# Optimization experiments

Measured on AMD Instinct MI355X. Metric: run time of the kernel, lower is better.

The kernel has to match this reference:

```python
import jax, jax.numpy as jnp
import numpy as np

N = 9
DIM = 2 ** N  # 512
RANGES = [1, 2, 3]  # PennyLane StronglyEntanglingLayers default: (l % (N-1)) + 1


def _cnot_mat(c, t):
    # CNOT on (control c, target t); wire 0 = most significant bit (default.qubit)
    idx = np.arange(DIM)
    bit = (idx >> (N - 1 - c)) & 1
    new = idx ^ (bit << (N - 1 - t))
    m = np.zeros((DIM, DIM), np.complex64)
    m[new, idx] = 1.0
    return m


def _layer_cnot_ring(r):
    # product of CNOT(i, (i+r) % N) applied for i = 0..N-1 (in circuit order)
    m = np.eye(DIM, dtype=np.complex64)
    for i in range(N):
        m = _cnot_mat(i, (i + r) % N) @ m
    return jnp.asarray(m)


_CNOT_LAYERS = [_layer_cnot_ring(r) for r in RANGES]

# PauliZ diagonal per wire: zd[w, k] = +1/-1 depending on bit w of basis index k
_ZDIAG = jnp.asarray(
    1.0 - 2.0 * (((np.arange(DIM)[None, :] >> (N - 1 - np.arange(N)[:, None])) & 1)),
    dtype=jnp.float32,
)


def _rot2x2(phi, theta, omega):
    # PennyLane Rot = RZ(omega) RY(theta) RZ(phi)
    phi = phi.astype(jnp.complex64)
    theta = theta.astype(jnp.complex64)
    omega = omega.astype(jnp.complex64)
    c = jnp.cos(theta / 2)
    s = jnp.sin(theta / 2)
    m00 = jnp.exp(-0.5j * (phi + omega)) * c
    m01 = -jnp.exp(0.5j * (phi - omega)) * s
    m10 = jnp.exp(-0.5j * (phi - omega)) * s
    m11 = jnp.exp(0.5j * (phi + omega)) * c
    return jnp.stack([jnp.stack([m00, m01]), jnp.stack([m10, m11])])


def _circuit_unitary(weights):
    # Full 512x512 unitary for the 3 StronglyEntanglingLayers (weight-dependent part)
    u = jnp.eye(DIM, dtype=jnp.complex64)
    for l in range(weights.shape[0]):
        rot = _rot2x2(weights[l, 0, 0], weights[l, 0, 1], weights[l, 0, 2])
        for w in range(1, N):
            rot = jnp.kron(rot, _rot2x2(weights[l, w, 0], weights[l, w, 1], weights[l, w, 2]))
        u = _CNOT_LAYERS[l] @ (rot @ u)
    return u


def _forward(x, weights):
    b = x.shape[0]
    # AngleEmbedding (RX) on |0>: per-qubit state [cos(t/2), -i sin(t/2)]
    half = x.astype(jnp.float32) / 2
    q = jnp.stack(
        [jnp.cos(half).astype(jnp.complex64), (-1j) * jnp.sin(half).astype(jnp.complex64)],
        axis=-1,
    )  # [B, 9, 2]
    s = q[:, 0, :]
    for w in range(1, N):  # batched kron across qubits -> [B, 512]
        s = (s[:, :, None] * q[:, w, None, :]).reshape(b, -1)
    u = _circuit_unitary(weights)
    psi = s @ u.T  # [B, 512]
    probs = psi.real ** 2 + psi.imag ** 2  # [B, 512] float32
    return probs @ _ZDIAG.T  # [B, 9] <Z_w> expectations


def setup_inputs() -> dict:
    key = jax.random.key(0)
    k1, k2 = jax.random.split(key)
    return {
        "x": jax.random.normal(k1, (32768, 9), dtype=jnp.float32),
        "weights": jax.random.normal(k2, (3, 9, 3), dtype=jnp.float32),
    }


def reference(x, weights):
    return _forward(x, weights).astype(jnp.float32)
```

## Files before the change

### kernel.cpp

```cpp
#include <hip/hip_runtime.h>
#include <hip/hip_fp16.h>


typedef float v2f __attribute__((ext_vector_type(2)));
typedef _Float16 v2h __attribute__((ext_vector_type(2)));

constexpr int pf(int l, int i) {
    const int r = l + 1; int j = i;
    for (int c = 0; c < 9; ++c) {
        const int bit = (j >> (8 - c)) & 1;
        const int t = (c + r) % 9;
        j ^= bit << (8 - t);
    }
    return j;
}

struct PMask { int m[2][9]; };
constexpr PMask make_pmask() {
    PMask pm{};
    for (int bd = 0; bd < 2; ++bd)
        for (int q = 0; q < 9; ++q) {
            const int img = pf(bd, 1 << q);
            for (int p = 0; p < 9; ++p)
                if ((img >> p) & 1) pm.m[bd][p] |= 1 << q;
        }
    return pm;
}
constexpr PMask PM = make_pmask();

struct Sig3 {
    int wbasis[6];
    int koff[8];
    int rimg[6];
};
constexpr Sig3 make_sig3(int l) {
    Sig3 out{};
    for (int limit = 2; limit <= 64; limit *= 2) {
        for (int idx = 0; idx < 720; ++idx) {
            int pool[6] = {3, 4, 5, 6, 7, 8};
            int perm[6] = {};
            int f = idx;
            const int fact[6] = {120, 24, 6, 2, 1, 1};
            int n = 6;
            for (int pos = 0; pos < 6; ++pos) {
                const int sel = f / fact[pos]; f %= fact[pos];
                perm[pos] = pool[sel];
                for (int m2 = sel; m2 + 1 < n; ++m2) pool[m2] = pool[m2 + 1];
                --n;
            }
            int img[9] = {0, 1, 2, perm[0], perm[1], perm[2],
                          perm[3], perm[4], perm[5]};
            int cnt[32] = {};
            bool ok = true;
            for (int L = 0; L < 64 && ok; ++L) {
                const int j = pf(l, L);
                int addr = 0;
                for (int bb = 0; bb < 9; ++bb)
                    if ((j >> bb) & 1) addr ^= 1 << img[bb];
                if (++cnt[addr & 31] > limit) ok = false;
            }
            if (ok) {
                for (int b2 = 0; b2 < 6; ++b2) {
                    const int j = pf(l, 1 << b2); int v = 0;
                    for (int bb = 0; bb < 9; ++bb)
                        if ((j >> bb) & 1) v ^= 1 << img[bb];
                    out.wbasis[b2] = v;
                }
                for (int k = 0; k < 8; ++k) {
                    const int j = pf(l, k << 6); int v = 0;
                    for (int bb = 0; bb < 9; ++bb)
                        if ((j >> bb) & 1) v ^= 1 << img[bb];
                    out.koff[k] = v;
                }
                for (int b2 = 0; b2 < 6; ++b2) out.rimg[b2] = img[3 + b2];
                return out;
            }
        }
    }
    return out;
}
constexpr Sig3 S3_0 = make_sig3(0);
constexpr Sig3 S3_1 = make_sig3(1);

#define PI_F    3.14159265358979323846f
#define INV2PI  0.15915494309189535f

static __device__ inline unsigned pack_rn(float x, float y) {
    const __half2 h = __floats2half2_rn(x, y);
    return *(const unsigned*)&h;
}

__global__ __launch_bounds__(512) void qtab_kernel(
        const float* __restrict__ wt, float* __restrict__ ws) {
    const int j = threadIdx.x;
    unsigned* wu = (unsigned*)ws;
    if (j < 27) {
        float s, c; __sincosf(0.5f * wt[j * 3 + 1], &s, &c);
        wu[j] = pack_rn(c, s);
    }
    #pragma unroll
    for (int bd = 0; bd < 2; ++bd) {
        float alpha = 0.0f;
        #pragma unroll
        for (int p = 0; p < 9; ++p) {
            const int w = 8 - p;
            const float om = wt[(bd * 9 + w) * 3 + 2];
            const float ph = wt[((bd + 1) * 9 + w) * 3 + 0];
            alpha += ((j >> p) & 1) ? 0.5f * om : -0.5f * om;
            alpha += (__popc(j & PM.m[bd][p]) & 1) ? 0.5f * ph : -0.5f * ph;
        }
        float sn, cs; __sincosf(alpha, &sn, &cs);
        wu[64 + bd * 512 + j] = pack_rn(cs, sn);
    }
    {
        float a = 0.0f;
        #pragma unroll
        for (int p = 0; p < 9; ++p) {
            const int w = 8 - p;
            const float phi = wt[w * 3 + 0];
            a += ((j >> p) & 1) ? (0.5f * phi - 0.5f * PI_F) : (-0.5f * phi);
        }
        float sn, cs; __sincosf(a, &sn, &cs);
        ((v2f*)(ws + 1088))[j] = (v2f){cs, sn};
    }
}

#define APPLY_GATE(G, KB)                                                     \
    {                                                                         \
        _Pragma("unroll")                                                     \
        for (int k0 = 0; k0 < 8; ++k0) if (!(k0 & (KB))) {                    \
            const int k1 = k0 | (KB);                                         \
            unsigned t;                                                       \
            asm("v_pk_mul_f16 %0, %1, %2 op_sel:[0,1] op_sel_hi:[1,1] "       \
                "neg_lo:[0,1] neg_hi:[0,1]"                                   \
                : "=v"(t) : "v"(a[k1]), "s"(G));               \
            asm("v_pk_mul_f16 %0, %0, %1 op_sel:[0,0] op_sel_hi:[1,0]"        \
                : "+v"(a[k1]) : "s"(G));                       \
            asm("v_pk_fma_f16 %0, %1, %2, %0 op_sel:[0,1,0] op_sel_hi:[1,1,1]"\
                : "+v"(a[k1]) : "v"(a[k0]), "s"(G));          \
            asm("v_pk_fma_f16 %0, %0, %1, %2 op_sel:[0,0,0] op_sel_hi:[1,0,1]"\
                : "+v"(a[k0]) : "s"(G), "v"(t));             \
        }                                                                     \
    }

__global__ __launch_bounds__(256) void qsim_kernel(
        const float* __restrict__ x,
        const float* __restrict__ tab,
        float* __restrict__ out,
        int batch) {
    __shared__ uint4 st4[4][128];

    const int tid  = threadIdx.x;
    const int wv   = tid >> 6;
    const int lane = tid & 63;
    const int b    = blockIdx.x * 4 + wv;
    if (b >= batch) return;
    const int bu   = __builtin_amdgcn_readfirstlane(b);

    unsigned* __restrict__ S  = (unsigned*)st4[wv];
    const uint4* __restrict__ S4 = st4[wv];
    const unsigned* __restrict__ tu = (const unsigned*)tab;
    const unsigned* __restrict__ D0 = tu + 64;
    const unsigned* __restrict__ D1 = tu + 576;
    const float4*  __restrict__ PH4 = (const float4*)(tab + 1088);

    float cx[9], sx[9];
    #pragma unroll
    for (int w = 0; w < 9; ++w) {
        const float rev = x[bu * 9 + w] * (0.5f * INV2PI);
        sx[w] = __builtin_amdgcn_sinf(rev);
        cx[w] = __builtin_amdgcn_cosf(rev);
    }
    float P = 1.0f;
    #pragma unroll
    for (int w = 0; w < 6; ++w)
        P *= ((lane >> (5 - w)) & 1) ? sx[w] : cx[w];

    float mk[8];
    {
        const float m0 = P * cx[6],  m1 = P * sx[6];
        const float m00 = m0 * cx[7], m01 = m0 * sx[7];
        const float m10 = m1 * cx[7], m11 = m1 * sx[7];
        mk[0] = m00 * cx[8]; mk[1] = m00 * sx[8];
        mk[2] = m01 * cx[8]; mk[3] = m01 * sx[8];
        mk[4] = m10 * cx[8]; mk[5] = m10 * sx[8];
        mk[6] = m11 * cx[8]; mk[7] = m11 * sx[8];
    }
    unsigned a[8];
    #pragma unroll
    for (int j2 = 0; j2 < 4; ++j2) {
        const float4 ph = PH4[(lane << 2) + j2];
        a[2 * j2]     = pack_rn(ph.x * mk[2 * j2],     ph.y * mk[2 * j2]);
        a[2 * j2 + 1] = pack_rn(ph.z * mk[2 * j2 + 1], ph.w * mk[2 * j2 + 1]);
    }

    const int wb1 = (lane & 31) | ((lane & 32) << 3);
    const int rb1 = ((lane & 7) << 5) | (lane & 0x18) | ((lane & 32) << 3);
    const int wb2 = ((lane >> 3) & 7) | ((lane & 3) << 3) | ((lane & 4) << 6);
    const int rb2 = ((lane & 3) << 3) | ((lane & 4) << 6) | ((lane & 0x38) << 2);
    int t3b[2], rb3[2];
    #pragma unroll
    for (int l = 0; l < 2; ++l) {
        int tb = 0, rb = 0;
        #pragma unroll
        for (int bb = 0; bb < 6; ++bb) {
            const int on = (lane >> bb) & 1;
            tb ^= on ? (l ? S3_1.wbasis[bb] : S3_0.wbasis[bb]) : 0;
            rb ^= on ? (1 << (l ? S3_1.rimg[bb] : S3_0.rimg[bb])) : 0;
        }
        t3b[l] = tb; rb3[l] = rb;
    }

    #pragma unroll
    for (int l = 0; l < 3; ++l) {
        unsigned g[9];
        #pragma unroll
        for (int q = 0; q < 9; ++q) g[q] = tu[l * 9 + q];

        APPLY_GATE(g[6], 4);
        APPLY_GATE(g[7], 2);
        APPLY_GATE(g[8], 1);

        #pragma unroll
        for (int k = 0; k < 8; ++k) S[wb1 + (k << 5)] = a[k];
        {
            const uint4 r0 = S4[(rb1 >> 2)];
            const uint4 r1 = S4[(rb1 >> 2) + 1];
            a[0] = r0.x; a[1] = r0.y; a[2] = r0.z; a[3] = r0.w;
            a[4] = r1.x; a[5] = r1.y; a[6] = r1.z; a[7] = r1.w;
        }

        APPLY_GATE(g[3], 4);
        APPLY_GATE(g[4], 2);
        APPLY_GATE(g[5], 1);

        #pragma unroll
        for (int k = 0; k < 8; ++k) S[wb2 + (k << 5)] = a[k];
        {
            const uint4 r0 = S4[(rb2 >> 2)];
            const uint4 r1 = S4[(rb2 >> 2) + 1];
            a[0] = r0.x; a[1] = r0.y; a[2] = r0.z; a[3] = r0.w;
            a[4] = r1.x; a[5] = r1.y; a[6] = r1.z; a[7] = r1.w;
        }

        APPLY_GATE(g[0], 4);
        APPLY_GATE(g[1], 2);
        APPLY_GATE(g[2], 1);

        if (l < 2) {
            const unsigned* __restrict__ D = (l == 0) ? D0 : D1;
            #pragma unroll
            for (int k = 0; k < 8; ++k) {
                const unsigned d = D[(k << 6) | lane];
                unsigned t;
                asm("v_pk_mul_f16 %0, %1, %2 op_sel:[1,1] op_sel_hi:[0,1] "
                    "neg_lo:[0,1]"
                    : "=v"(t) : "v"(a[k]), "v"(d));
                asm("v_pk_fma_f16 %0, %1, %2, %3 op_sel:[0,0,0] op_sel_hi:[1,0,1]"
                    : "=v"(a[k]) : "v"(a[k]), "v"(d), "v"(t));
            }
            #pragma unroll
            for (int k = 0; k < 8; ++k)
                S[t3b[l] ^ (l ? S3_1.koff[k] : S3_0.koff[k])] = a[k];
            {
                const uint4 r0 = S4[(rb3[l] >> 2)];
                const uint4 r1 = S4[(rb3[l] >> 2) + 1];
                a[0] = r0.x; a[1] = r0.y; a[2] = r0.z; a[3] = r0.w;
                a[4] = r1.x; a[5] = r1.y; a[6] = r1.z; a[7] = r1.w;
            }
        }
    }

    float A0 = 0.f, A1 = 0.f, A2 = 0.f, A3 = 0.f;
    #pragma unroll
    for (int k = 0; k < 8; ++k) {
#if __has_builtin(__builtin_amdgcn_fdot2)
        v2h h, hn;
        { unsigned u = a[k];               h = *(const v2h*)&u; }
        { unsigned un = a[k] ^ 0x80008000u; hn = *(const v2h*)&un; }
        A0 = __builtin_amdgcn_fdot2(h, h, A0, false);
        A1 = __builtin_amdgcn_fdot2(h, (k & 4) ? hn : h, A1, false);
        A2 = __builtin_amdgcn_fdot2(h, (k & 2) ? hn : h, A2, false);
        A3 = __builtin_amdgcn_fdot2(h, (k & 1) ? hn : h, A3, false);
#else
        const __half2 h = *(const __half2*)&a[k];
        const float2 f = __half22float2(h);
        const float p = f.x * f.x + f.y * f.y;
        A0 += p;
        A1 += (k & 4) ? -p : p;
        A2 += (k & 2) ? -p : p;
        A3 += (k & 1) ? -p : p;
#endif
    }
    v2f F01 = (v2f){A0, A1};
    v2f F23 = (v2f){A2, A3};

    #pragma unroll
    for (int d = 1; d < 64; d <<= 1) {
        const float sg1 = (lane & d) ? -1.0f : 1.0f;
        const v2f sgn = (v2f){sg1, sg1};
        v2f p01, p23;
        p01.x = __shfl_xor(F01.x, d, 64);  p01.y = __shfl_xor(F01.y, d, 64);
        p23.x = __shfl_xor(F23.x, d, 64);  p23.y = __shfl_xor(F23.y, d, 64);
        F01 = F01 * sgn + p01;
        F23 = F23 * sgn + p23;
    }
    float* Sf = (float*)S;
    Sf[2 * lane]           = F01.x;
    Sf[2 * lane + 1]       = F01.y;
    Sf[128 + 2 * lane]     = F23.x;
    Sf[128 + 2 * lane + 1] = F23.y;
    if (lane < 9) {
        const int idx = (lane == 0) ? 72  : (lane == 1) ? 36  : (lane == 2) ? 18
                      : (lane == 3) ? 65  : (lane == 4) ? 160 : (lane == 5) ? 145
                      : (lane == 6) ? 73  : (lane == 7) ? 164 : 147;
        out[bu * 9 + lane] = Sf[idx];
    }
}

extern "C" void kernel_launch(void* const* d_in, const int* in_sizes, int n_in,
                              void* d_out, int out_size, void* d_ws, size_t ws_size,
                              hipStream_t stream) {
    const float* x  = (const float*)d_in[0];
    const float* wt = (const float*)d_in[1];
    float* out = (float*)d_out;
    const int batch = in_sizes[0] / 9;
    float* ws = (float*)d_ws;

    hipLaunchKernelGGL(qtab_kernel, dim3(1), dim3(512), 0, stream, wt, ws);
    hipLaunchKernelGGL(qsim_kernel, dim3((batch + 3) / 4), dim3(256), 0, stream,
                       x, ws, out, batch);
}
```

Measured before the change: 99.58 us.

## Process two batch rows per wavefront with interleaved gate and transpose phases

Each wavefront now simulates two batch samples, interleaving gate application of one state with the LDS transpose of the other to expose instruction-level parallelism. The diagonal phase tables are loaded into registers once per wave and reused for both samples, and the grid is halved. This raises register pressure and halves the number of waves, which may reduce occupancy or latency hiding.

```diff
diff --git a/kernel.cpp b/kernel.cpp
--- a/kernel.cpp
+++ b/kernel.cpp
@@ -125,7 +125,7 @@
     }
 }
 
-#define APPLY_GATE(G, KB)                                                     \
+#define APPLY_GATE(ar, G, KB)                                                 \
     {                                                                         \
         _Pragma("unroll")                                                     \
         for (int k0 = 0; k0 < 8; ++k0) if (!(k0 & (KB))) {                    \
@@ -133,13 +133,79 @@
             unsigned t;                                                       \
             asm("v_pk_mul_f16 %0, %1, %2 op_sel:[0,1] op_sel_hi:[1,1] "       \
                 "neg_lo:[0,1] neg_hi:[0,1]"                                   \
-                : "=v"(t) : "v"(a[k1]), "s"(G));               \
+                : "=v"(t) : "v"(ar[k1]), "s"(G));              \
             asm("v_pk_mul_f16 %0, %0, %1 op_sel:[0,0] op_sel_hi:[1,0]"        \
-                : "+v"(a[k1]) : "s"(G));                       \
+                : "+v"(ar[k1]) : "s"(G));                      \
             asm("v_pk_fma_f16 %0, %1, %2, %0 op_sel:[0,1,0] op_sel_hi:[1,1,1]"\
-                : "+v"(a[k1]) : "v"(a[k0]), "s"(G));          \
+                : "+v"(ar[k1]) : "v"(ar[k0]), "s"(G));        \
             asm("v_pk_fma_f16 %0, %0, %1, %2 op_sel:[0,0,0] op_sel_hi:[1,0,1]"\
-                : "+v"(a[k0]) : "s"(G), "v"(t));             \
+                : "+v"(ar[k0]) : "s"(G), "v"(t));            \
+        }                                                                     \
+    }
+
+#define XPOSE(ar, wb, rb)                                                     \
+    {                                                                         \
+        _Pragma("unroll")                                                     \
+        for (int k = 0; k < 8; ++k) S[(wb) + (k << 5)] = ar[k];               \
+        const uint4 r0 = S4[((rb) >> 2)];                                     \
+        const uint4 r1 = S4[((rb) >> 2) + 1];                                 \
+        ar[0] = r0.x; ar[1] = r0.y; ar[2] = r0.z; ar[3] = r0.w;               \
+        ar[4] = r1.x; ar[5] = r1.y; ar[6] = r1.z; ar[7] = r1.w;               \
+    }
+
+#define XPOSE3(ar, ll)                                                        \
+    {                                                                         \
+        _Pragma("unroll")                                                     \
+        for (int k = 0; k < 8; ++k)                                           \
+            S[t3b[ll] ^ ((ll) ? S3_1.koff[k] : S3_0.koff[k])] = ar[k];        \
+        const uint4 r0 = S4[(rb3[ll] >> 2)];                                  \
+        const uint4 r1 = S4[(rb3[ll] >> 2) + 1];                              \
+        ar[0] = r0.x; ar[1] = r0.y; ar[2] = r0.z; ar[3] = r0.w;               \
+        ar[4] = r1.x; ar[5] = r1.y; ar[6] = r1.z; ar[7] = r1.w;               \
+    }
+
+#define CMUL_D(ar, dv)                                                        \
+    {                                                                         \
+        _Pragma("unroll")                                                     \
+        for (int k = 0; k < 8; ++k) {                                         \
+            const unsigned d = dv[k];                                         \
+            unsigned t;                                                       \
+            asm("v_pk_mul_f16 %0, %1, %2 op_sel:[1,1] op_sel_hi:[0,1] "       \
+                "neg_lo:[0,1]"                                                \
+                : "=v"(t) : "v"(ar[k]), "v"(d));                              \
+            asm("v_pk_fma_f16 %0, %1, %2, %3 op_sel:[0,0,0] op_sel_hi:[1,0,1]"\
+                : "=v"(ar[k]) : "v"(ar[k]), "v"(d), "v"(t));                  \
+        }                                                                     \
+    }
+
+#define INIT_STATE(ar, row)                                                   \
+    {                                                                         \
+        float cx[9], sx[9];                                                   \
+        _Pragma("unroll")                                                     \
+        for (int w = 0; w < 9; ++w) {                                         \
+            const float rev = x[(row) * 9 + w] * (0.5f * INV2PI);             \
+            sx[w] = __builtin_amdgcn_sinf(rev);                               \
+            cx[w] = __builtin_amdgcn_cosf(rev);                               \
+        }                                                                     \
+        float P = 1.0f;                                                       \
+        _Pragma("unroll")                                                     \
+        for (int w = 0; w < 6; ++w)                                           \
+            P *= ((lane >> (5 - w)) & 1) ? sx[w] : cx[w];                     \
+        float mk[8];                                                          \
+        {                                                                     \
+            const float m0 = P * cx[6],  m1 = P * sx[6];                      \
+            const float m00 = m0 * cx[7], m01 = m0 * sx[7];                   \
+            const float m10 = m1 * cx[7], m11 = m1 * sx[7];                   \
+            mk[0] = m00 * cx[8]; mk[1] = m00 * sx[8];                         \
+            mk[2] = m01 * cx[8]; mk[3] = m01 * sx[8];                         \
+            mk[4] = m10 * cx[8]; mk[5] = m10 * sx[8];                         \
+            mk[6] = m11 * cx[8]; mk[7] = m11 * sx[8];                         \
+        }                                                                     \
+        _Pragma("unroll")                                                     \
+        for (int j2 = 0; j2 < 4; ++j2) {                                      \
+            const float4 ph = PH4[(lane << 2) + j2];                          \
+            ar[2 * j2]     = pack_rn(ph.x * mk[2 * j2],     ph.y * mk[2 * j2]);\
+            ar[2 * j2 + 1] = pack_rn(ph.z * mk[2 * j2 + 1], ph.w * mk[2 * j2 + 1]);\
         }                                                                     \
     }
 
@@ -153,9 +219,10 @@
     const int tid  = threadIdx.x;
     const int wv   = tid >> 6;
     const int lane = tid & 63;
-    const int b    = blockIdx.x * 4 + wv;
-    if (b >= batch) return;
-    const int bu   = __builtin_amdgcn_readfirstlane(b);
+    const int b0   = (blockIdx.x * 4 + wv) * 2;
+    if (b0 >= batch) return;
+    const int bu   = __builtin_amdgcn_readfirstlane(b0);
+    const int buB  = (bu + 1 < batch) ? (bu + 1) : bu;
 
     unsigned* __restrict__ S  = (unsigned*)st4[wv];
     const uint4* __restrict__ S4 = st4[wv];
@@ -164,35 +231,13 @@
     const unsigned* __restrict__ D1 = tu + 576;
     const float4*  __restrict__ PH4 = (const float4*)(tab + 1088);
 
-    float cx[9], sx[9];
-    #pragma unroll
-    for (int w = 0; w < 9; ++w) {
-        const float rev = x[bu * 9 + w] * (0.5f * INV2PI);
-        sx[w] = __builtin_amdgcn_sinf(rev);
-        cx[w] = __builtin_amdgcn_cosf(rev);
-    }
-    float P = 1.0f;
-    #pragma unroll
-    for (int w = 0; w < 6; ++w)
-        P *= ((lane >> (5 - w)) & 1) ? sx[w] : cx[w];
-
-    float mk[8];
-    {
-        const float m0 = P * cx[6],  m1 = P * sx[6];
-        const float m00 = m0 * cx[7], m01 = m0 * sx[7];
-        const float m10 = m1 * cx[7], m11 = m1 * sx[7];
-        mk[0] = m00 * cx[8]; mk[1] = m00 * sx[8];
-        mk[2] = m01 * cx[8]; mk[3] = m01 * sx[8];
-        mk[4] = m10 * cx[8]; mk[5] = m10 * sx[8];
-        mk[6] = m11 * cx[8]; mk[7] = m11 * sx[8];
-    }
-    unsigned a[8];
-    #pragma unroll
-    for (int j2 = 0; j2 < 4; ++j2) {
-        const float4 ph = PH4[(lane << 2) + j2];
-        a[2 * j2]     = pack_rn(ph.x * mk[2 * j2],     ph.y * mk[2 * j2]);
-        a[2 * j2 + 1] = pack_rn(ph.z * mk[2 * j2 + 1], ph.w * mk[2 * j2 + 1]);
-    }
+    unsigned aA[8], aB[8];
+    INIT_STATE(aA, bu)
+    INIT_STATE(aB, buB)
+
+    unsigned d0v[8], d1v[8];
+    #pragma unroll
+    for (int k = 0; k < 8; ++k) d0v[k] = D0[(k << 6) | lane];
 
     const int wb1 = (lane & 31) | ((lane & 32) << 3);
     const int rb1 = ((lane & 7) << 5) | (lane & 0x18) | ((lane & 32) << 3);
@@ -216,105 +261,118 @@
         unsigned g[9];
         #pragma unroll
         for (int q = 0; q < 9; ++q) g[q] = tu[l * 9 + q];
-
-        APPLY_GATE(g[6], 4);
-        APPLY_GATE(g[7], 2);
-        APPLY_GATE(g[8], 1);
-
-        #pragma unroll
-        for (int k = 0; k < 8; ++k) S[wb1 + (k << 5)] = a[k];
-        {
-            const uint4 r0 = S4[(rb1 >> 2)];
-            const uint4 r1 = S4[(rb1 >> 2) + 1];
-            a[0] = r0.x; a[1] = r0.y; a[2] = r0.z; a[3] = r0.w;
-            a[4] = r1.x; a[5] = r1.y; a[6] = r1.z; a[7] = r1.w;
-        }
-
-        APPLY_GATE(g[3], 4);
-        APPLY_GATE(g[4], 2);
-        APPLY_GATE(g[5], 1);
-
-        #pragma unroll
-        for (int k = 0; k < 8; ++k) S[wb2 + (k << 5)] = a[k];
-        {
-            const uint4 r0 = S4[(rb2 >> 2)];
-            const uint4 r1 = S4[(rb2 >> 2) + 1];
-            a[0] = r0.x; a[1] = r0.y; a[2] = r0.z; a[3] = r0.w;
-            a[4] = r1.x; a[5] = r1.y; a[6] = r1.z; a[7] = r1.w;
-        }
-
-        APPLY_GATE(g[0], 4);
-        APPLY_GATE(g[1], 2);
-        APPLY_GATE(g[2], 1);
-
+        if (l == 1) {
+            #pragma unroll
+            for (int k = 0; k < 8; ++k) d1v[k] = D1[(k << 6) | lane];
+        }
+
+        APPLY_GATE(aA, g[6], 4);
+        APPLY_GATE(aA, g[7], 2);
+        APPLY_GATE(aA, g[8], 1);
+        XPOSE(aA, wb1, rb1);
+        APPLY_GATE(aB, g[6], 4);
+        APPLY_GATE(aB, g[7], 2);
+        APPLY_GATE(aB, g[8], 1);
+        XPOSE(aB, wb1, rb1);
+
+        APPLY_GATE(aA, g[3], 4);
+        APPLY_GATE(aA, g[4], 2);
+        APPLY_GATE(aA, g[5], 1);
+        XPOSE(aA, wb2, rb2);
+        APPLY_GATE(aB, g[3], 4);
+        APPLY_GATE(aB, g[4], 2);
+        APPLY_GATE(aB, g[5], 1);
+        XPOSE(aB, wb2, rb2);
+
+        APPLY_GATE(aA, g[0], 4);
+        APPLY_GATE(aA, g[1], 2);
+        APPLY_GATE(aA, g[2], 1);
         if (l < 2) {
-            const unsigned* __restrict__ D = (l == 0) ? D0 : D1;
-            #pragma unroll
-            for (int k = 0; k < 8; ++k) {
-                const unsigned d = D[(k << 6) | lane];
-                unsigned t;
-                asm("v_pk_mul_f16 %0, %1, %2 op_sel:[1,1] op_sel_hi:[0,1] "
-                    "neg_lo:[0,1]"
-                    : "=v"(t) : "v"(a[k]), "v"(d));
-                asm("v_pk_fma_f16 %0, %1, %2, %3 op_sel:[0,0,0] op_sel_hi:[1,0,1]"
-                    : "=v"(a[k]) : "v"(a[k]), "v"(d), "v"(t));
-            }
-            #pragma unroll
-            for (int k = 0; k < 8; ++k)
-                S[t3b[l] ^ (l ? S3_1.koff[k] : S3_0.koff[k])] = a[k];
-            {
-                const uint4 r0 = S4[(rb3[l] >> 2)];
-                const uint4 r1 = S4[(rb3[l] >> 2) + 1];
-                a[0] = r0.x; a[1] = r0.y; a[2] = r0.z; a[3] = r0.w;
-                a[4] = r1.x; a[5] = r1.y; a[6] = r1.z; a[7] = r1.w;
-            }
+            if (l == 0) { CMUL_D(aA, d0v); } else { CMUL_D(aA, d1v); }
+            XPOSE3(aA, l);
+        }
+        APPLY_GATE(aB, g[0], 4);
+        APPLY_GATE(aB, g[1], 2);
+        APPLY_GATE(aB, g[2], 1);
+        if (l < 2) {
+            if (l == 0) { CMUL_D(aB, d0v); } else { CMUL_D(aB, d1v); }
+            XPOSE3(aB, l);
         }
     }
 
     float A0 = 0.f, A1 = 0.f, A2 = 0.f, A3 = 0.f;
+    float B0 = 0.f, B1 = 0.f, B2 = 0.f, B3 = 0.f;
     #pragma unroll
     for (int k = 0; k < 8; ++k) {
 #if __has_builtin(__builtin_amdgcn_fdot2)
         v2h h, hn;
-        { unsigned u = a[k];               h = *(const v2h*)&u; }
-        { unsigned un = a[k] ^ 0x80008000u; hn = *(const v2h*)&un; }
+        { unsigned u = aA[k];               h = *(const v2h*)&u; }
+        { unsigned un = aA[k] ^ 0x80008000u; hn = *(const v2h*)&un; }
         A0 = __builtin_amdgcn_fdot2(h, h, A0, false);
         A1 = __builtin_amdgcn_fdot2(h, (k & 4) ? hn : h, A1, false);
         A2 = __builtin_amdgcn_fdot2(h, (k & 2) ? hn : h, A2, false);
         A3 = __builtin_amdgcn_fdot2(h, (k & 1) ? hn : h, A3, false);
+        { unsigned u = aB[k];               h = *(const v2h*)&u; }
+        { unsigned un = aB[k] ^ 0x80008000u; hn = *(const v2h*)&un; }
+        B0 = __builtin_amdgcn_fdot2(h, h, B0, false);
+        B1 = __builtin_amdgcn_fdot2(h, (k & 4) ? hn : h, B1, false);
+        B2 = __builtin_amdgcn_fdot2(h, (k & 2) ? hn : h, B2, false);
+        B3 = __builtin_amdgcn_fdot2(h, (k & 1) ? hn : h, B3, false);
 #else
-        const __half2 h = *(const __half2*)&a[k];
-        const float2 f = __half22float2(h);
-        const float p = f.x * f.x + f.y * f.y;
-        A0 += p;
-        A1 += (k & 4) ? -p : p;
-        A2 += (k & 2) ? -p : p;
-        A3 += (k & 1) ? -p : p;
+        {
+            const __half2 h = *(const __half2*)&aA[k];
+            const float2 f = __half22float2(h);
+            const float p = f.x * f.x + f.y * f.y;
+            A0 += p;
+            A1 += (k & 4) ? -p : p;
+            A2 += (k & 2) ? -p : p;
+            A3 += (k & 1) ? -p : p;
+        }
+        {
+            const __half2 h = *(const __half2*)&aB[k];
+            const float2 f = __half22float2(h);
+            const float p = f.x * f.x + f.y * f.y;
+            B0 += p;
+            B1 += (k & 4) ? -p : p;
+            B2 += (k & 2) ? -p : p;
+            B3 += (k & 1) ? -p : p;
+        }
 #endif
     }
-    v2f F01 = (v2f){A0, A1};
-    v2f F23 = (v2f){A2, A3};
+    v2f FA01 = (v2f){A0, A1};
+    v2f FA23 = (v2f){A2, A3};
+    v2f FB01 = (v2f){B0, B1};
+    v2f FB23 = (v2f){B2, B3};
 
     #pragma unroll
     for (int d = 1; d < 64; d <<= 1) {
         const float sg1 = (lane & d) ? -1.0f : 1.0f;
         const v2f sgn = (v2f){sg1, sg1};
-        v2f p01, p23;
-        p01.x = __shfl_xor(F01.x, d, 64);  p01.y = __shfl_xor(F01.y, d, 64);
-        p23.x = __shfl_xor(F23.x, d, 64);  p23.y = __shfl_xor(F23.y, d, 64);
-        F01 = F01 * sgn + p01;
-        F23 = F23 * sgn + p23;
+        v2f pA01, pA23, pB01, pB23;
+        pA01.x = __shfl_xor(FA01.x, d, 64);  pA01.y = __shfl_xor(FA01.y, d, 64);
+        pA23.x = __shfl_xor(FA23.x, d, 64);  pA23.y = __shfl_xor(FA23.y, d, 64);
+        pB01.x = __shfl_xor(FB01.x, d, 64);  pB01.y = __shfl_xor(FB01.y, d, 64);
+        pB23.x = __shfl_xor(FB23.x, d, 64);  pB23.y = __shfl_xor(FB23.y, d, 64);
+        FA01 = FA01 * sgn + pA01;
+        FA23 = FA23 * sgn + pA23;
+        FB01 = FB01 * sgn + pB01;
+        FB23 = FB23 * sgn + pB23;
     }
     float* Sf = (float*)S;
-    Sf[2 * lane]           = F01.x;
-    Sf[2 * lane + 1]       = F01.y;
-    Sf[128 + 2 * lane]     = F23.x;
-    Sf[128 + 2 * lane + 1] = F23.y;
+    Sf[2 * lane]           = FA01.x;
+    Sf[2 * lane + 1]       = FA01.y;
+    Sf[128 + 2 * lane]     = FA23.x;
+    Sf[128 + 2 * lane + 1] = FA23.y;
+    Sf[256 + 2 * lane]     = FB01.x;
+    Sf[256 + 2 * lane + 1] = FB01.y;
+    Sf[384 + 2 * lane]     = FB23.x;
+    Sf[384 + 2 * lane + 1] = FB23.y;
     if (lane < 9) {
         const int idx = (lane == 0) ? 72  : (lane == 1) ? 36  : (lane == 2) ? 18
                       : (lane == 3) ? 65  : (lane == 4) ? 160 : (lane == 5) ? 145
                       : (lane == 6) ? 73  : (lane == 7) ? 164 : 147;
         out[bu * 9 + lane] = Sf[idx];
+        if (bu + 1 < batch) out[(bu + 1) * 9 + lane] = Sf[256 + idx];
     }
 }
 
@@ -328,6 +386,6 @@
     float* ws = (float*)d_ws;
 
     hipLaunchKernelGGL(qtab_kernel, dim3(1), dim3(512), 0, stream, wt, ws);
-    hipLaunchKernelGGL(qsim_kernel, dim3((batch + 3) / 4), dim3(256), 0, stream,
+    hipLaunchKernelGGL(qsim_kernel, dim3((batch + 7) / 8), dim3(256), 0, stream,
                        x, ws, out, batch);
 }
```

Measured after the change: 97.73 us. No clear change (-1.9%).
